# Kernel tuning notes

Hardware: AMD Instinct MI355X
Metric: run time of the kernel (lower is better)

Reference implementation:

```python
import jax, jax.numpy as jnp
import numpy as np

B, D, C, T = 2, 1024, 256, 32
H = 8
F = C // H
E = 1024  # time_embed_dim
GROUPS = 32
SCALE = F ** -0.5


def group_norm(x, scale, bias):
    # x: [B, D, C, T]; GroupNorm(32, C) over (channels-in-group, T)
    b, d, c, t = x.shape
    xg = x.reshape(b, d, GROUPS, c // GROUPS, t)
    m = xg.mean(axis=(3, 4), keepdims=True)
    v = xg.var(axis=(3, 4), keepdims=True)
    xn = ((xg - m) * jax.lax.rsqrt(v + 1e-5)).reshape(b, d, c, t)
    return xn * scale[None, None, :, None] + bias[None, None, :, None]


def rpe_R(temb, pairwise, dw, db, tw, tb, ow, ob):
    # pairwise: [B, T, T] int -> R: [B, T, T, H, F]
    pd = pairwise.astype(jnp.float32)
    dist_embs = jnp.stack([
        jnp.log1p(jnp.maximum(pd, 0.0)),
        jnp.log1p(jnp.maximum(-pd, 0.0)),
        (pairwise == 0).astype(jnp.float32),
    ], axis=-1)  # [B, T, T, 3]
    emb = (temb @ tw.T + tb)[:, :, None, :] + (dist_embs @ dw.T + db)  # [B,T,T,C]
    r = jax.nn.silu(emb) @ ow.T + ob
    return r.reshape(r.shape[0], r.shape[1], r.shape[2], H, F)


def setup_inputs() -> dict:
    key = jax.random.key(0)
    ks = jax.random.split(key, 20)
    s = 0.02
    inp = {
        "x": jax.random.normal(ks[0], (B, D, C, T), jnp.float32),
        "temb": jax.random.normal(ks[1], (B, T, E), jnp.float32),
        "norm_scale": jnp.ones((C,), jnp.float32),
        "norm_bias": jnp.zeros((C,), jnp.float32),
        "qkv_w": jax.random.normal(ks[2], (3 * C, C), jnp.float32) * s,
        "qkv_b": jnp.zeros((3 * C,), jnp.float32),
        "proj_w": jax.random.normal(ks[3], (C, C), jnp.float32) * s,
        "proj_b": jnp.zeros((C,), jnp.float32),
        # stacked RPE params for (q, k, v) nets
        "rpe_dist_w": jax.random.normal(ks[4], (3, C, 3), jnp.float32) * s,
        "rpe_dist_b": jnp.zeros((3, C), jnp.float32),
        "rpe_time_w": jax.random.normal(ks[5], (3, C, E), jnp.float32) * s,
        "rpe_time_b": jnp.zeros((3, C), jnp.float32),
        "rpe_out_w": jax.random.normal(ks[6], (3, C, C), jnp.float32) * s,
        "rpe_out_b": jax.random.normal(ks[7], (3, C), jnp.float32) * s,
        "frame_indices": jnp.sort(jax.random.randint(ks[8], (B, T), 0, 100), axis=-1),
    }
    return inp


def reference(x, temb, norm_scale, norm_bias, qkv_w, qkv_b, proj_w, proj_b,
              rpe_dist_w, rpe_dist_b, rpe_time_w, rpe_time_b, rpe_out_w, rpe_out_b,
              frame_indices):
    xn = group_norm(x, norm_scale, norm_bias)          # [B,D,C,T]
    xt = jnp.einsum('BDCT->BDTC', xn)                  # [B,D,T,C]
    qkv = (xt @ qkv_w.T + qkv_b).reshape(B, D, T, 3, H, F)
    qkv = jnp.einsum('BDTtHF->tBDHTF', qkv)
    q, k, v = qkv[0] * SCALE, qkv[1], qkv[2]           # [B,D,H,T,F]

    attn = jnp.einsum('bdhtf,bdhsf->bdhts', q, k)

    pairwise = frame_indices[:, :, None] - frame_indices[:, None, :]  # [B,T,T]
    R_q = rpe_R(temb, pairwise, rpe_dist_w[0], rpe_dist_b[0], rpe_time_w[0], rpe_time_b[0], rpe_out_w[0], rpe_out_b[0])
    R_k = rpe_R(temb, pairwise, rpe_dist_w[1], rpe_dist_b[1], rpe_time_w[1], rpe_time_b[1], rpe_out_w[1], rpe_out_b[1])
    R_v = rpe_R(temb, pairwise, rpe_dist_w[2], rpe_dist_b[2], rpe_time_w[2], rpe_time_b[2], rpe_out_w[2], rpe_out_b[2])

    attn = attn + jnp.einsum('bdhtf,btshf->bdhts', q, R_k)
    # rpe_q: forward_qk on (k*scale) then transpose last two dims
    attn = attn + jnp.einsum('bdhtf,btshf->bdhts', k * SCALE, R_q).swapaxes(-1, -2)

    attn = jax.nn.softmax(attn.astype(jnp.float32), axis=-1).astype(attn.dtype)

    out = jnp.einsum('bdhts,bdhsf->bdhtf', attn, v)
    out = out + jnp.einsum('bdhts,btshf->bdhtf', attn, R_v)

    out = jnp.einsum('BDHTF->BDTHF', out).reshape(B, D, T, C)
    out = out @ proj_w.T + proj_b
    y = xt + out                                       # residual on post-norm x (as in source)
    return jnp.einsum('BDTC->BDCT', y)
```

## Files before the change

kernel.cpp:

```cpp
#include <hip/hip_runtime.h>

#define BB 2
#define DD 1024
#define CC 256
#define TT 32
#define HH 8
#define FF 32
#define EE 1024
#define SCALE 0.17677669529663687f

typedef unsigned short u16;
typedef unsigned int u32;
typedef __attribute__((ext_vector_type(8))) short s8v;
typedef __attribute__((ext_vector_type(4))) float f32x4;

static __device__ __forceinline__ float u2f(u16 u) {
  return __uint_as_float(((u32)u) << 16);
}
static __device__ __forceinline__ u16 f2u(float f) {
  u32 x = __float_as_uint(f);
  x += 0x7fffu + ((x >> 16) & 1u);
  return (u16)(x >> 16);
}
static __device__ __forceinline__ float dot2bf(u32 a, u32 b, float c) {
  float d;
  asm("v_dot2_f32_bf16 %0, %1, %2, %3" : "=v"(d) : "v"(a), "v"(b), "v"(c));
  return d;
}
#define D2(acc, a, b) acc = dot2bf(a, b, acc)

static __device__ __forceinline__ float logits_r(
    const u16* kr,
    uint4 r0, uint4 r1, uint4 r2, uint4 r3,
    uint4 r4, uint4 r5, uint4 r6, uint4 r7,
    uint4 q0, uint4 q1, uint4 q2, uint4 q3) {
  uint4 k0 = *(const uint4*)(kr + 0);
  uint4 k1 = *(const uint4*)(kr + 8);
  uint4 k2 = *(const uint4*)(kr + 16);
  uint4 k3 = *(const uint4*)(kr + 24);
  float xq = 0.f, xr = 0.f, xk = 0.f;
  D2(xq, q0.x, k0.x); D2(xq, q0.y, k0.y); D2(xq, q0.z, k0.z); D2(xq, q0.w, k0.w);
  D2(xq, q1.x, k1.x); D2(xq, q1.y, k1.y); D2(xq, q1.z, k1.z); D2(xq, q1.w, k1.w);
  D2(xq, q2.x, k2.x); D2(xq, q2.y, k2.y); D2(xq, q2.z, k2.z); D2(xq, q2.w, k2.w);
  D2(xq, q3.x, k3.x); D2(xq, q3.y, k3.y); D2(xq, q3.z, k3.z); D2(xq, q3.w, k3.w);
  D2(xr, q0.x, r0.x); D2(xr, q0.y, r0.y); D2(xr, q0.z, r0.z); D2(xr, q0.w, r0.w);
  D2(xr, q1.x, r1.x); D2(xr, q1.y, r1.y); D2(xr, q1.z, r1.z); D2(xr, q1.w, r1.w);
  D2(xr, q2.x, r2.x); D2(xr, q2.y, r2.y); D2(xr, q2.z, r2.z); D2(xr, q2.w, r2.w);
  D2(xr, q3.x, r3.x); D2(xr, q3.y, r3.y); D2(xr, q3.z, r3.z); D2(xr, q3.w, r3.w);
  D2(xk, k0.x, r4.x); D2(xk, k0.y, r4.y); D2(xk, k0.z, r4.z); D2(xk, k0.w, r4.w);
  D2(xk, k1.x, r5.x); D2(xk, k1.y, r5.y); D2(xk, k1.z, r5.z); D2(xk, k1.w, r5.w);
  D2(xk, k2.x, r6.x); D2(xk, k2.y, r6.y); D2(xk, k2.z, r6.z); D2(xk, k2.w, r6.w);
  D2(xk, k3.x, r7.x); D2(xk, k3.y, r7.y); D2(xk, k3.z, r7.z); D2(xk, k3.w, r7.w);
  return xq + xr + xk;
}

static __device__ __forceinline__ float pv_r(
    uint4 p0, uint4 p1, uint4 p2, uint4 p3,
    const u16* vr, uint4 r0, uint4 r1, uint4 r2, uint4 r3) {
  uint4 v0 = *(const uint4*)(vr + 0),  v1 = *(const uint4*)(vr + 8);
  uint4 v2 = *(const uint4*)(vr + 16), v3 = *(const uint4*)(vr + 24);
  float o = 0.f;
  D2(o, p0.x, v0.x); D2(o, p0.y, v0.y); D2(o, p0.z, v0.z); D2(o, p0.w, v0.w);
  D2(o, p1.x, v1.x); D2(o, p1.y, v1.y); D2(o, p1.z, v1.z); D2(o, p1.w, v1.w);
  D2(o, p2.x, v2.x); D2(o, p2.y, v2.y); D2(o, p2.z, v2.z); D2(o, p2.w, v2.w);
  D2(o, p3.x, v3.x); D2(o, p3.y, v3.y); D2(o, p3.z, v3.z); D2(o, p3.w, v3.w);
  D2(o, p0.x, r0.x); D2(o, p0.y, r0.y); D2(o, p0.z, r0.z); D2(o, p0.w, r0.w);
  D2(o, p1.x, r1.x); D2(o, p1.y, r1.y); D2(o, p1.z, r1.z); D2(o, p1.w, r1.w);
  D2(o, p2.x, r2.x); D2(o, p2.y, r2.y); D2(o, p2.z, r2.z); D2(o, p2.w, r2.w);
  D2(o, p3.x, r3.x); D2(o, p3.y, r3.y); D2(o, p3.z, r3.z); D2(o, p3.w, r3.w);
  return o;
}

#define LOADROW8(P, v0, v1, v2, v3, v4, v5, v6, v7)                      \
  v0 = *(const uint4*)((P) + 0);  v1 = *(const uint4*)((P) + 8);         \
  v2 = *(const uint4*)((P) + 16); v3 = *(const uint4*)((P) + 24);        \
  v4 = *(const uint4*)((P) + 32); v5 = *(const uint4*)((P) + 40);        \
  v6 = *(const uint4*)((P) + 48); v7 = *(const uint4*)((P) + 56);
#define LOADROW4(P, v0, v1, v2, v3)                                      \
  v0 = *(const uint4*)((P) + 0);  v1 = *(const uint4*)((P) + 8);         \
  v2 = *(const uint4*)((P) + 16); v3 = *(const uint4*)((P) + 24);

__global__ void k_prep(const float* __restrict__ qw, const float* __restrict__ pw,
                       const float* __restrict__ ow, const float* __restrict__ tw,
                       u16* __restrict__ wpk2, u16* __restrict__ ppk,
                       u16* __restrict__ opk, float* __restrict__ twT) {
  int id = blockIdx.x * 256 + threadIdx.x;
  if (id < 24576) {
    int lane = id & 63, ks = (id >> 6) & 7, tile = id >> 9;
    int hh = tile / 6, r = tile % 6, sec = r >> 1, nt = r & 1;
    int nrow = sec * 256 + hh * 32 + nt * 16 + (lane & 15);
    int k = ks * 32 + (lane >> 4) * 8;
    const float* src = qw + (size_t)nrow * 256 + k;
    u16* dst = wpk2 + (size_t)id * 8;
#pragma unroll
    for (int e = 0; e < 8; ++e) dst[e] = f2u(src[e]);
  } else if (id < 32768) {
    int j = id - 24576;
    int lane = j & 63, ks = (j >> 6) & 7, nt = j >> 9;
    int row = nt * 16 + (lane & 15);
    int k = ks * 32 + (lane >> 4) * 8;
    const float* src = pw + (size_t)row * 256 + k;
    u16* dst = ppk + (size_t)j * 8;
#pragma unroll
    for (int e = 0; e < 8; ++e) dst[e] = f2u(src[e]);
  } else if (id < 57344) {
    int j = id - 32768;
    int lane = j & 63, ks = (j >> 6) & 7, g = j >> 9;
    int n = g >> 4, ntg = g & 15;
    int row = ntg * 16 + (lane & 15);
    int k = ks * 32 + (lane >> 4) * 8;
    const float* src = ow + ((size_t)n * 256 + row) * 256 + k;
    u16* dst = opk + (size_t)j * 8;
#pragma unroll
    for (int e = 0; e < 8; ++e) dst[e] = f2u(src[e]);
  } else {
    int j = id - 57344;
    int n = j >> 16, r = j & 65535;
    int e = r >> 6, c0 = (r & 63) * 4;
    float4 v;
    v.x = tw[((size_t)n * 256 + c0 + 0) * 1024 + e];
    v.y = tw[((size_t)n * 256 + c0 + 1) * 1024 + e];
    v.z = tw[((size_t)n * 256 + c0 + 2) * 1024 + e];
    v.w = tw[((size_t)n * 256 + c0 + 3) * 1024 + e];
    *(float4*)(twT + (size_t)n * 262144 + (size_t)e * 256 + c0) = v;
  }
}

__global__ __launch_bounds__(256) void k_tpe(
    const float* __restrict__ temb, const float* __restrict__ twT,
    const float* __restrict__ tb, const float* __restrict__ dw,
    const float* __restrict__ db, const int* __restrict__ fidx,
    u16* __restrict__ E) {
  int bid = blockIdx.x;
  int t = bid & 31, b = (bid >> 5) & 1, n = bid >> 6;
  __shared__ float st[EE];
  __shared__ int sfi[TT];
  for (int e = threadIdx.x; e < EE; e += 256)
    st[e] = temb[((size_t)b * TT + t) * EE + e];
  if (threadIdx.x < TT) sfi[threadIdx.x] = fidx[b * TT + threadIdx.x];
  __syncthreads();
  int c = threadIdx.x;
  const float* wp = twT + (size_t)n * 262144 + c;
  float a0 = 0.f, a1 = 0.f, a2 = 0.f, a3 = 0.f;
  for (int e = 0; e < EE; e += 4) {
    a0 += st[e + 0] * wp[(size_t)(e + 0) * 256];
    a1 += st[e + 1] * wp[(size_t)(e + 1) * 256];
    a2 += st[e + 2] * wp[(size_t)(e + 2) * 256];
    a3 += st[e + 3] * wp[(size_t)(e + 3) * 256];
  }
  float base = a0 + a1 + a2 + a3 + tb[n * 256 + c] + db[n * 256 + c];
  float dw0 = dw[(n * 256 + c) * 3 + 0];
  float dw1 = dw[(n * 256 + c) * 3 + 1];
  float dw2 = dw[(n * 256 + c) * 3 + 2];
  int ft = sfi[t];
  u16* erow = E + ((size_t)n * 2048 + b * 1024 + t * 32) * 256 + c;
  for (int s = 0; s < TT; ++s) {
    int pd = ft - sfi[s];
    float d0 = log1pf((float)(pd > 0 ? pd : 0));
    float d1 = log1pf((float)(pd < 0 ? -pd : 0));
    float d2 = (pd == 0) ? 1.f : 0.f;
    float e = base + d0 * dw0 + d1 * dw1 + d2 * dw2;
    float se = e / (1.f + expf(-e));
    erow[(size_t)s * 256] = f2u(se);
  }
}

__global__ __launch_bounds__(256) void k_rgemm(
    const u16* __restrict__ E, const u16* __restrict__ opk,
    const float* __restrict__ ob,
    u16* __restrict__ RKQ, u16* __restrict__ Rv) {
  int bid = blockIdx.x;
  int n = bid >> 6, rem = bid & 63;
  int mblk = rem >> 1, nblk = rem & 1;
  int tid = threadIdx.x;
  int w = tid >> 6, lane = tid & 63;
  int l15 = lane & 15, l4 = lane >> 4;
  size_t rowbase = (size_t)n * 2048 + mblk * 64;

  f32x4 acc[2][4];
#pragma unroll
  for (int i = 0; i < 2; ++i) {
    int ntg = nblk * 8 + w * 2 + i;
    float ov = ob[n * 256 + ntg * 16 + l15];
#pragma unroll
    for (int mt = 0; mt < 4; ++mt) acc[i][mt] = (f32x4){ov, ov, ov, ov};
  }
  for (int ks = 0; ks < 8; ++ks) {
    s8v a[4];
#pragma unroll
    for (int mt = 0; mt < 4; ++mt)
      a[mt] = *(const s8v*)(E + (rowbase + mt * 16 + l15) * 256 + ks * 32 + l4 * 8);
#pragma unroll
    for (int i = 0; i < 2; ++i) {
      int ntg = nblk * 8 + w * 2 + i;
      s8v bf = *(const s8v*)(opk + (((size_t)(n * 16 + ntg) * 8 + ks) * 64 + lane) * 8);
#pragma unroll
      for (int mt = 0; mt < 4; ++mt)
        acc[i][mt] = __builtin_amdgcn_mfma_f32_16x16x32_bf16(a[mt], bf, acc[i][mt], 0, 0, 0);
    }
  }
#pragma unroll
  for (int i = 0; i < 2; ++i) {
    int cc = (nblk * 8 + w * 2 + i) * 16 + l15;
    int hh = cc >> 5, f = cc & 31;
#pragma unroll
    for (int mt = 0; mt < 4; ++mt)
#pragma unroll
      for (int r = 0; r < 4; ++r) {
        int rloc = mblk * 64 + mt * 16 + l4 * 4 + r;
        int bb2 = rloc >> 10, tt = (rloc >> 5) & 31, ss = rloc & 31;
        size_t bh = (size_t)(bb2 * 8 + hh);
        float v = acc[i][mt][r];
        if (n == 0)      RKQ[(bh * 1024 + ss * 32 + tt) * 64 + 32 + f] = f2u(v * SCALE);
        else if (n == 1) RKQ[(bh * 1024 + tt * 32 + ss) * 64 + f] = f2u(v);
        else             Rv[((bh * 32 + tt) * 32 + f) * 32 + ss] = f2u(v);
      }
  }
}

__global__ __launch_bounds__(256, 4) void k_gn(
    const float* __restrict__ x, const float* __restrict__ nsc,
    const float* __restrict__ nbi, u16* __restrict__ pun) {
  int bid = blockIdx.x;
  int xcd = bid & 7, jj = bid >> 3;
  int b = xcd >> 2;
  int d = (xcd & 3) * 256 + jj;
  const int tid = threadIdx.x;
  __shared__ u16 xt[TT][264];
  const size_t xbase = ((size_t)(b * DD + d)) * 8192;
  u16* xnp = pun + xbase * 2 + 8192;
  {
    const int c0 = tid >> 3, tq = tid & 7;
    for (int c = c0; c < CC; c += 32) {
      float4 v = *(const float4*)(x + xbase + (size_t)c * TT + tq * 4);
      xt[tq * 4 + 0][c] = f2u(v.x);
      xt[tq * 4 + 1][c] = f2u(v.y);
      xt[tq * 4 + 2][c] = f2u(v.z);
      xt[tq * 4 + 3][c] = f2u(v.w);
    }
  }
  __syncthreads();
  {
    const int c = tid;
    float s = 0.f, s2 = 0.f;
    for (int t = 0; t < TT; ++t) { float v = u2f(xt[t][c]); s += v; s2 += v * v; }
    s += __shfl_xor(s, 1); s2 += __shfl_xor(s2, 1);
    s += __shfl_xor(s, 2); s2 += __shfl_xor(s2, 2);
    s += __shfl_xor(s, 4); s2 += __shfl_xor(s2, 4);
    const float mean = s * (1.f / 256.f);
    const float var = s2 * (1.f / 256.f) - mean * mean;
    const float rs = rsqrtf(var + 1e-5f);
    const float scv = nsc[c] * rs;
    const float biv = nbi[c] - mean * scv;
    for (int t = 0; t < TT; ++t) xt[t][c] = f2u(u2f(xt[t][c]) * scv + biv);
  }
  __syncthreads();
#pragma unroll
  for (int it = 0; it < 4; ++it) {
    int u = it * 256 + tid;
    int t = u >> 5, c = (u & 31) * 8;
    *(uint4*)(xnp + (size_t)u * 8) = *(const uint4*)&xt[t][c];
  }
}

__global__ __launch_bounds__(256, 3) void k_attn(
    u16* __restrict__ pun, const u16* __restrict__ wpk2,
    const float* __restrict__ qkb,
    const u16* __restrict__ RKQ, const u16* __restrict__ Rv) {
  int bid = blockIdx.x;
  int xcd = bid & 7, i5 = bid >> 3;
  int b = xcd >> 2;
  int h = i5 & 7;
  int dg = (xcd & 3) * 64 + (i5 >> 3);
  int d0 = dg * 4;
  const int tid = threadIdx.x;
  __shared__ u16 xsbuf[32 * 264];
  __shared__ u16 qs[4][32][40];
  __shared__ u16 ks_[4][32][40];
  __shared__ u16 vT[4][32][40];
#define XS_(r, c)   xsbuf[(r) * 264 + (c)]
#define ATSP(d, t)  (xsbuf + ((d) * 32 + (t)) * 40)

  const int w = tid >> 6, lane = tid & 63;
  const int l15 = lane & 15, l4 = lane >> 4;
  const int t = tid >> 3, j = tid & 7;
  const size_t bh = (size_t)(b * 8 + h);
  const u16* rp0 = RKQ + (bh * 1024 + (size_t)t * 32 + j) * 64;
  const u16* rv0 = Rv + ((bh * 32 + (size_t)t) * 32 + j) * 32;

  u16* slot0 = pun + ((size_t)(b * DD + d0)) * 16384;

  const u16* xp0 = slot0 + 8192;
  uint4 xr0 = *(const uint4*)(xp0 + (size_t)tid * 8);
  uint4 xr1 = *(const uint4*)(xp0 + (size_t)(256 + tid) * 8);
  uint4 xr2 = *(const uint4*)(xp0 + (size_t)(512 + tid) * 8);
  uint4 xr3 = *(const uint4*)(xp0 + (size_t)(768 + tid) * 8);

  for (int d = 0; d < 4; ++d) {
    *(uint4*)&XS_((tid >> 5), (tid & 31) * 8) = xr0;
    *(uint4*)&XS_(8 + (tid >> 5), (tid & 31) * 8) = xr1;
    *(uint4*)&XS_(16 + (tid >> 5), (tid & 31) * 8) = xr2;
    *(uint4*)&XS_(24 + (tid >> 5), (tid & 31) * 8) = xr3;
    __syncthreads();
    if (d < 3) {
      const u16* nx = slot0 + (size_t)(d + 1) * 16384 + 8192;
      xr0 = *(const uint4*)(nx + (size_t)tid * 8);
      xr1 = *(const uint4*)(nx + (size_t)(256 + tid) * 8);
      xr2 = *(const uint4*)(nx + (size_t)(512 + tid) * 8);
      xr3 = *(const uint4*)(nx + (size_t)(768 + tid) * 8);
    }
#pragma unroll
    for (int i = 0; i < 3; ++i) {
      const int u = w * 3 + i;
      const int sec = u >> 2;
      const int nt = (u >> 1) & 1;
      const int mh = u & 1;
      f32x4 acc = {0.f, 0.f, 0.f, 0.f};
      const u16* wb = wpk2 + ((size_t)((h * 6 + sec * 2 + nt) * 8) * 64 + lane) * 8;
      for (int ks = 0; ks < 8; ++ks) {
        s8v a = *(const s8v*)&XS_(mh * 16 + l15, ks * 32 + l4 * 8);
        s8v bf = *(const s8v*)(wb + (size_t)ks * 512);
        acc = __builtin_amdgcn_mfma_f32_16x16x32_bf16(a, bf, acc, 0, 0, 0);
      }
      const int f = nt * 16 + l15;
      const float bias = qkb[sec * 256 + h * 32 + f];
#pragma unroll
      for (int r = 0; r < 4; ++r) {
        const int tt = mh * 16 + l4 * 4 + r;
        const float val = acc[r] + bias;
        if (sec == 0)      qs[d][tt][f] = f2u(val * SCALE);
        else if (sec == 1) ks_[d][tt][f] = f2u(val);
        else               vT[d][f][tt] = f2u(val);
      }
    }
    __syncthreads();
  }

  uint4 q[4][4];
#pragma unroll
  for (int d = 0; d < 4; ++d) {
    q[d][0] = *(const uint4*)&qs[d][t][0];
    q[d][1] = *(const uint4*)&qs[d][t][8];
    q[d][2] = *(const uint4*)&qs[d][t][16];
    q[d][3] = *(const uint4*)&qs[d][t][24];
  }
  float a[4][4];
  uint4 A0, A1, A2, A3, A4, A5, A6, A7;
  uint4 B0, B1, B2, B3, B4, B5, B6, B7;
  LOADROW8(rp0,          A0, A1, A2, A3, A4, A5, A6, A7)
  LOADROW8(rp0 + 8 * 64, B0, B1, B2, B3, B4, B5, B6, B7)
#pragma unroll
  for (int d = 0; d < 4; ++d)
    a[d][0] = logits_r(&ks_[d][j][0], A0, A1, A2, A3, A4, A5, A6, A7,
                       q[d][0], q[d][1], q[d][2], q[d][3]);
  LOADROW8(rp0 + 16 * 64, A0, A1, A2, A3, A4, A5, A6, A7)
#pragma unroll
  for (int d = 0; d < 4; ++d)
    a[d][1] = logits_r(&ks_[d][j + 8][0], B0, B1, B2, B3, B4, B5, B6, B7,
                       q[d][0], q[d][1], q[d][2], q[d][3]);
  LOADROW8(rp0 + 24 * 64, B0, B1, B2, B3, B4, B5, B6, B7)
#pragma unroll
  for (int d = 0; d < 4; ++d)
    a[d][2] = logits_r(&ks_[d][j + 16][0], A0, A1, A2, A3, A4, A5, A6, A7,
                       q[d][0], q[d][1], q[d][2], q[d][3]);
#pragma unroll
  for (int d = 0; d < 4; ++d)
    a[d][3] = logits_r(&ks_[d][j + 24][0], B0, B1, B2, B3, B4, B5, B6, B7,
                       q[d][0], q[d][1], q[d][2], q[d][3]);

#pragma unroll
  for (int d = 0; d < 4; ++d) {
    float mx = fmaxf(fmaxf(a[d][0], a[d][1]), fmaxf(a[d][2], a[d][3]));
    mx = fmaxf(mx, __shfl_xor(mx, 1));
    mx = fmaxf(mx, __shfl_xor(mx, 2));
    mx = fmaxf(mx, __shfl_xor(mx, 4));
    float e0 = __expf(a[d][0] - mx), e1 = __expf(a[d][1] - mx);
    float e2 = __expf(a[d][2] - mx), e3 = __expf(a[d][3] - mx);
    float sum = e0 + e1 + e2 + e3;
    sum += __shfl_xor(sum, 1);
    sum += __shfl_xor(sum, 2);
    sum += __shfl_xor(sum, 4);
    const float inv = 1.f / sum;
    u16* ap = ATSP(d, t);
    ap[j]      = f2u(e0 * inv);
    ap[j + 8]  = f2u(e1 * inv);
    ap[j + 16] = f2u(e2 * inv);
    ap[j + 24] = f2u(e3 * inv);
  }

  uint4 p[4][4];
#pragma unroll
  for (int d = 0; d < 4; ++d) {
    const u16* ap = ATSP(d, t);
    p[d][0] = *(const uint4*)(ap + 0);
    p[d][1] = *(const uint4*)(ap + 8);
    p[d][2] = *(const uint4*)(ap + 16);
    p[d][3] = *(const uint4*)(ap + 24);
  }
  float o[4][4];
  uint4 VA0, VA1, VA2, VA3, VB0, VB1, VB2, VB3;
  LOADROW4(rv0,          VA0, VA1, VA2, VA3)
  LOADROW4(rv0 + 8 * 32, VB0, VB1, VB2, VB3)
#pragma unroll
  for (int d = 0; d < 4; ++d)
    o[d][0] = pv_r(p[d][0], p[d][1], p[d][2], p[d][3], &vT[d][j][0],
                   VA0, VA1, VA2, VA3);
  LOADROW4(rv0 + 16 * 32, VA0, VA1, VA2, VA3)
#pragma unroll
  for (int d = 0; d < 4; ++d)
    o[d][1] = pv_r(p[d][0], p[d][1], p[d][2], p[d][3], &vT[d][j + 8][0],
                   VB0, VB1, VB2, VB3);
  LOADROW4(rv0 + 24 * 32, VB0, VB1, VB2, VB3)
#pragma unroll
  for (int d = 0; d < 4; ++d)
    o[d][2] = pv_r(p[d][0], p[d][1], p[d][2], p[d][3], &vT[d][j + 16][0],
                   VA0, VA1, VA2, VA3);
#pragma unroll
  for (int d = 0; d < 4; ++d)
    o[d][3] = pv_r(p[d][0], p[d][1], p[d][2], p[d][3], &vT[d][j + 24][0],
                   VB0, VB1, VB2, VB3);

#pragma unroll
  for (int d = 0; d < 4; ++d) {
    u16* op = slot0 + (size_t)d * 16384 + (size_t)t * 256 + h * 32 + j;
    op[0]  = f2u(o[d][0]);
    op[8]  = f2u(o[d][1]);
    op[16] = f2u(o[d][2]);
    op[24] = f2u(o[d][3]);
  }
#undef XS_
#undef ATSP
}

__global__ __launch_bounds__(256, 4) void k_proj(
    u16* __restrict__ pun, const u16* __restrict__ ppk,
    const float* __restrict__ pb, float* __restrict__ out) {
  int bid = blockIdx.x;
  int xcd = bid & 7, jj = bid >> 3;
  int b = xcd >> 2;
  int d = (xcd & 3) * 256 + jj;
  const int tid = threadIdx.x;
  __shared__ u16 obuf[32][264];
  __shared__ u16 xs[32][264];
  const size_t nbase = ((size_t)(b * DD + d)) * 8192;
  u16* slot = pun + nbase * 2;
#pragma unroll
  for (int it = 0; it < 4; ++it) {
    int u = it * 256 + tid;
    int t = u >> 5, c = (u & 31) * 8;
    *(uint4*)&obuf[t][c] = *(const uint4*)(slot + (size_t)u * 8);
    *(uint4*)&xs[t][c]   = *(const uint4*)(slot + 8192 + (size_t)u * 8);
  }
  __syncthreads();

  const int w = tid >> 6, lane = tid & 63;
  const int l15 = lane & 15, l4 = lane >> 4;
  f32x4 pacc[4][2];
#pragma unroll
  for (int i = 0; i < 4; ++i) {
    pacc[i][0] = (f32x4){0.f, 0.f, 0.f, 0.f};
    pacc[i][1] = (f32x4){0.f, 0.f, 0.f, 0.f};
  }
  for (int ks = 0; ks < 8; ++ks) {
    s8v a0 = *(const s8v*)&obuf[l15][ks * 32 + l4 * 8];
    s8v a1 = *(const s8v*)&obuf[16 + l15][ks * 32 + l4 * 8];
#pragma unroll
    for (int i = 0; i < 4; ++i) {
      s8v bf = *(const s8v*)(ppk + ((size_t)((w * 4 + i) * 8 + ks) * 64 + lane) * 8);
      pacc[i][0] = __builtin_amdgcn_mfma_f32_16x16x32_bf16(a0, bf, pacc[i][0], 0, 0, 0);
      pacc[i][1] = __builtin_amdgcn_mfma_f32_16x16x32_bf16(a1, bf, pacc[i][1], 0, 0, 0);
    }
  }
#pragma unroll
  for (int i = 0; i < 4; ++i) {
    const int co = (w * 4 + i) * 16 + l15;
    const float pbv = pb[co];
#pragma unroll
    for (int mt = 0; mt < 2; ++mt) {
      const int t0 = mt * 16 + l4 * 4;
      float4 sv;
      sv.x = pacc[i][mt][0] + u2f(xs[t0 + 0][co]) + pbv;
      sv.y = pacc[i][mt][1] + u2f(xs[t0 + 1][co]) + pbv;
      sv.z = pacc[i][mt][2] + u2f(xs[t0 + 2][co]) + pbv;
      sv.w = pacc[i][mt][3] + u2f(xs[t0 + 3][co]) + pbv;
      *(float4*)(out + nbase + (size_t)co * TT + t0) = sv;
    }
  }
}

extern "C" void kernel_launch(void* const* d_in, const int* in_sizes, int n_in,
                              void* d_out, int out_size, void* d_ws, size_t ws_size,
                              hipStream_t stream) {
  const float* x      = (const float*)d_in[0];
  const float* temb   = (const float*)d_in[1];
  const float* nsc    = (const float*)d_in[2];
  const float* nbi    = (const float*)d_in[3];
  const float* qkv_w  = (const float*)d_in[4];
  const float* qkv_b  = (const float*)d_in[5];
  const float* proj_w = (const float*)d_in[6];
  const float* proj_b = (const float*)d_in[7];
  const float* dw     = (const float*)d_in[8];
  const float* db     = (const float*)d_in[9];
  const float* tw     = (const float*)d_in[10];
  const float* tb     = (const float*)d_in[11];
  const float* ow     = (const float*)d_in[12];
  const float* ob     = (const float*)d_in[13];
  const int*   fidx   = (const int*)d_in[14];
  float* out = (float*)d_out;
  u16* pun = (u16*)d_out;

  float* twT = (float*)d_ws;
  u16* wpk2 = (u16*)(twT + 786432);
  u16* ppk  = wpk2 + 196608;
  u16* opk  = ppk + 65536;
  u16* E    = opk + 196608;
  u16* RKQ  = E + 1572864;
  u16* Rv   = RKQ + 1048576;

  k_prep<<<992, 256, 0, stream>>>(qkv_w, proj_w, ow, tw, wpk2, ppk, opk, twT);
  k_tpe<<<192, 256, 0, stream>>>(temb, twT, tb, dw, db, fidx, E);
  k_rgemm<<<192, 256, 0, stream>>>(E, opk, ob, RKQ, Rv);
  k_gn<<<2048, 256, 0, stream>>>(x, nsc, nbi, pun);
  k_attn<<<4096, 256, 0, stream>>>(pun, wpk2, qkv_b, RKQ, Rv);
  k_proj<<<2048, 256, 0, stream>>>(pun, ppk, proj_b, out);
}
```

Before: 249.0 us.

## Fuse prep, time-embedding and groupnorm kernels; prefetch RPE rows in attention

Merges weight packing, the time-embedding projection and groupnorm into a single launch partitioned by block index. This removes two launches and lets the independent stages run concurrently. The time-embedding dot product now reads tw directly with coalesced row-wise float4 loads and a shuffle reduction, which drops the transposed twT copy and its workspace. In the attention kernel, the first RPE row loads are issued before the QKV projection loop, pinned in registers with empty asm barriers, and q and p are reloaded from shared memory instead of held in registers, trading register pressure for LDS traffic.

```diff
diff --git a/kernel.cpp b/kernel.cpp
--- a/kernel.cpp
+++ b/kernel.cpp
@@ -28,16 +28,16 @@
   return d;
 }
 #define D2(acc, a, b) acc = dot2bf(a, b, acc)
-
-static __device__ __forceinline__ float logits_r(
-    const u16* kr,
+#define KEEP4(v) asm volatile("" : "+v"(v.x), "+v"(v.y), "+v"(v.z), "+v"(v.w))
+
+static __device__ __forceinline__ float logits_q(
+    const u16* kr, const u16* qr,
     uint4 r0, uint4 r1, uint4 r2, uint4 r3,
-    uint4 r4, uint4 r5, uint4 r6, uint4 r7,
-    uint4 q0, uint4 q1, uint4 q2, uint4 q3) {
-  uint4 k0 = *(const uint4*)(kr + 0);
-  uint4 k1 = *(const uint4*)(kr + 8);
-  uint4 k2 = *(const uint4*)(kr + 16);
-  uint4 k3 = *(const uint4*)(kr + 24);
+    uint4 r4, uint4 r5, uint4 r6, uint4 r7) {
+  uint4 q0 = *(const uint4*)(qr + 0),  q1 = *(const uint4*)(qr + 8);
+  uint4 q2 = *(const uint4*)(qr + 16), q3 = *(const uint4*)(qr + 24);
+  uint4 k0 = *(const uint4*)(kr + 0),  k1 = *(const uint4*)(kr + 8);
+  uint4 k2 = *(const uint4*)(kr + 16), k3 = *(const uint4*)(kr + 24);
   float xq = 0.f, xr = 0.f, xk = 0.f;
   D2(xq, q0.x, k0.x); D2(xq, q0.y, k0.y); D2(xq, q0.z, k0.z); D2(xq, q0.w, k0.w);
   D2(xq, q1.x, k1.x); D2(xq, q1.y, k1.y); D2(xq, q1.z, k1.z); D2(xq, q1.w, k1.w);
@@ -54,9 +54,11 @@
   return xq + xr + xk;
 }
 
-static __device__ __forceinline__ float pv_r(
-    uint4 p0, uint4 p1, uint4 p2, uint4 p3,
-    const u16* vr, uint4 r0, uint4 r1, uint4 r2, uint4 r3) {
+static __device__ __forceinline__ float pv_q(
+    const u16* pr, const u16* vr,
+    uint4 r0, uint4 r1, uint4 r2, uint4 r3) {
+  uint4 p0 = *(const uint4*)(pr + 0),  p1 = *(const uint4*)(pr + 8);
+  uint4 p2 = *(const uint4*)(pr + 16), p3 = *(const uint4*)(pr + 24);
   uint4 v0 = *(const uint4*)(vr + 0),  v1 = *(const uint4*)(vr + 8);
   uint4 v2 = *(const uint4*)(vr + 16), v3 = *(const uint4*)(vr + 24);
   float o = 0.f;
@@ -79,89 +81,135 @@
 #define LOADROW4(P, v0, v1, v2, v3)                                      \
   v0 = *(const uint4*)((P) + 0);  v1 = *(const uint4*)((P) + 8);         \
   v2 = *(const uint4*)((P) + 16); v3 = *(const uint4*)((P) + 24);
-
-__global__ void k_prep(const float* __restrict__ qw, const float* __restrict__ pw,
-                       const float* __restrict__ ow, const float* __restrict__ tw,
-                       u16* __restrict__ wpk2, u16* __restrict__ ppk,
-                       u16* __restrict__ opk, float* __restrict__ twT) {
-  int id = blockIdx.x * 256 + threadIdx.x;
-  if (id < 24576) {
-    int lane = id & 63, ks = (id >> 6) & 7, tile = id >> 9;
-    int hh = tile / 6, r = tile % 6, sec = r >> 1, nt = r & 1;
-    int nrow = sec * 256 + hh * 32 + nt * 16 + (lane & 15);
-    int k = ks * 32 + (lane >> 4) * 8;
-    const float* src = qw + (size_t)nrow * 256 + k;
-    u16* dst = wpk2 + (size_t)id * 8;
-#pragma unroll
-    for (int e = 0; e < 8; ++e) dst[e] = f2u(src[e]);
-  } else if (id < 32768) {
-    int j = id - 24576;
-    int lane = j & 63, ks = (j >> 6) & 7, nt = j >> 9;
-    int row = nt * 16 + (lane & 15);
-    int k = ks * 32 + (lane >> 4) * 8;
-    const float* src = pw + (size_t)row * 256 + k;
-    u16* dst = ppk + (size_t)j * 8;
-#pragma unroll
-    for (int e = 0; e < 8; ++e) dst[e] = f2u(src[e]);
-  } else if (id < 57344) {
-    int j = id - 32768;
-    int lane = j & 63, ks = (j >> 6) & 7, g = j >> 9;
-    int n = g >> 4, ntg = g & 15;
-    int row = ntg * 16 + (lane & 15);
-    int k = ks * 32 + (lane >> 4) * 8;
-    const float* src = ow + ((size_t)n * 256 + row) * 256 + k;
-    u16* dst = opk + (size_t)j * 8;
-#pragma unroll
-    for (int e = 0; e < 8; ++e) dst[e] = f2u(src[e]);
+#define KEEP8(a0,a1,a2,a3,a4,a5,a6,a7) \
+  KEEP4(a0); KEEP4(a1); KEEP4(a2); KEEP4(a3); KEEP4(a4); KEEP4(a5); KEEP4(a6); KEEP4(a7)
+
+__global__ __launch_bounds__(256, 4) void k_f0(
+    const float* __restrict__ x, const float* __restrict__ nsc,
+    const float* __restrict__ nbi, u16* __restrict__ pun,
+    const float* __restrict__ qw, const float* __restrict__ pw,
+    const float* __restrict__ ow, const float* __restrict__ tw,
+    const float* __restrict__ temb, const float* __restrict__ tb,
+    const float* __restrict__ dw, const float* __restrict__ db,
+    const int* __restrict__ fidx,
+    u16* __restrict__ wpk2, u16* __restrict__ ppk, u16* __restrict__ opk,
+    u16* __restrict__ E) {
+  const int bid = blockIdx.x;
+  const int tid = threadIdx.x;
+  __shared__ u16 xt[TT][264];
+  __shared__ float st[EE];
+  __shared__ float base_s[CC];
+  __shared__ int sfi[TT];
+
+  if (bid < 2048) {
+    int xcd = bid & 7, jj = bid >> 3;
+    int b = xcd >> 2;
+    int d = (xcd & 3) * 256 + jj;
+    const size_t xbase = ((size_t)(b * DD + d)) * 8192;
+    u16* xnp = pun + xbase * 2 + 8192;
+    {
+      const int c0 = tid >> 3, tq = tid & 7;
+      for (int c = c0; c < CC; c += 32) {
+        float4 v = *(const float4*)(x + xbase + (size_t)c * TT + tq * 4);
+        xt[tq * 4 + 0][c] = f2u(v.x);
+        xt[tq * 4 + 1][c] = f2u(v.y);
+        xt[tq * 4 + 2][c] = f2u(v.z);
+        xt[tq * 4 + 3][c] = f2u(v.w);
+      }
+    }
+    __syncthreads();
+    {
+      const int c = tid;
+      float s = 0.f, s2 = 0.f;
+      for (int t = 0; t < TT; ++t) { float v = u2f(xt[t][c]); s += v; s2 += v * v; }
+      s += __shfl_xor(s, 1); s2 += __shfl_xor(s2, 1);
+      s += __shfl_xor(s, 2); s2 += __shfl_xor(s2, 2);
+      s += __shfl_xor(s, 4); s2 += __shfl_xor(s2, 4);
+      const float mean = s * (1.f / 256.f);
+      const float var = s2 * (1.f / 256.f) - mean * mean;
+      const float rs = rsqrtf(var + 1e-5f);
+      const float scv = nsc[c] * rs;
+      const float biv = nbi[c] - mean * scv;
+      for (int t = 0; t < TT; ++t) xt[t][c] = f2u(u2f(xt[t][c]) * scv + biv);
+    }
+    __syncthreads();
+#pragma unroll
+    for (int it = 0; it < 4; ++it) {
+      int u = it * 256 + tid;
+      int t = u >> 5, c = (u & 31) * 8;
+      *(uint4*)(xnp + (size_t)u * 8) = *(const uint4*)&xt[t][c];
+    }
+  } else if (bid < 2272) {
+    int id = (bid - 2048) * 256 + tid;
+    if (id < 24576) {
+      int lane = id & 63, ks = (id >> 6) & 7, tile = id >> 9;
+      int hh = tile / 6, r = tile % 6, sec = r >> 1, nt = r & 1;
+      int nrow = sec * 256 + hh * 32 + nt * 16 + (lane & 15);
+      int k = ks * 32 + (lane >> 4) * 8;
+      const float* src = qw + (size_t)nrow * 256 + k;
+      u16* dst = wpk2 + (size_t)id * 8;
+#pragma unroll
+      for (int e = 0; e < 8; ++e) dst[e] = f2u(src[e]);
+    } else if (id < 32768) {
+      int j = id - 24576;
+      int lane = j & 63, ks = (j >> 6) & 7, nt = j >> 9;
+      int row = nt * 16 + (lane & 15);
+      int k = ks * 32 + (lane >> 4) * 8;
+      const float* src = pw + (size_t)row * 256 + k;
+      u16* dst = ppk + (size_t)j * 8;
+#pragma unroll
+      for (int e = 0; e < 8; ++e) dst[e] = f2u(src[e]);
+    } else {
+      int j = id - 32768;
+      int lane = j & 63, ks = (j >> 6) & 7, g = j >> 9;
+      int n = g >> 4, ntg = g & 15;
+      int row = ntg * 16 + (lane & 15);
+      int k = ks * 32 + (lane >> 4) * 8;
+      const float* src = ow + ((size_t)n * 256 + row) * 256 + k;
+      u16* dst = opk + (size_t)j * 8;
+#pragma unroll
+      for (int e = 0; e < 8; ++e) dst[e] = f2u(src[e]);
+    }
   } else {
-    int j = id - 57344;
-    int n = j >> 16, r = j & 65535;
-    int e = r >> 6, c0 = (r & 63) * 4;
-    float4 v;
-    v.x = tw[((size_t)n * 256 + c0 + 0) * 1024 + e];
-    v.y = tw[((size_t)n * 256 + c0 + 1) * 1024 + e];
-    v.z = tw[((size_t)n * 256 + c0 + 2) * 1024 + e];
-    v.w = tw[((size_t)n * 256 + c0 + 3) * 1024 + e];
-    *(float4*)(twT + (size_t)n * 262144 + (size_t)e * 256 + c0) = v;
-  }
-}
-
-__global__ __launch_bounds__(256) void k_tpe(
-    const float* __restrict__ temb, const float* __restrict__ twT,
-    const float* __restrict__ tb, const float* __restrict__ dw,
-    const float* __restrict__ db, const int* __restrict__ fidx,
-    u16* __restrict__ E) {
-  int bid = blockIdx.x;
-  int t = bid & 31, b = (bid >> 5) & 1, n = bid >> 6;
-  __shared__ float st[EE];
-  __shared__ int sfi[TT];
-  for (int e = threadIdx.x; e < EE; e += 256)
-    st[e] = temb[((size_t)b * TT + t) * EE + e];
-  if (threadIdx.x < TT) sfi[threadIdx.x] = fidx[b * TT + threadIdx.x];
-  __syncthreads();
-  int c = threadIdx.x;
-  const float* wp = twT + (size_t)n * 262144 + c;
-  float a0 = 0.f, a1 = 0.f, a2 = 0.f, a3 = 0.f;
-  for (int e = 0; e < EE; e += 4) {
-    a0 += st[e + 0] * wp[(size_t)(e + 0) * 256];
-    a1 += st[e + 1] * wp[(size_t)(e + 1) * 256];
-    a2 += st[e + 2] * wp[(size_t)(e + 2) * 256];
-    a3 += st[e + 3] * wp[(size_t)(e + 3) * 256];
-  }
-  float base = a0 + a1 + a2 + a3 + tb[n * 256 + c] + db[n * 256 + c];
-  float dw0 = dw[(n * 256 + c) * 3 + 0];
-  float dw1 = dw[(n * 256 + c) * 3 + 1];
-  float dw2 = dw[(n * 256 + c) * 3 + 2];
-  int ft = sfi[t];
-  u16* erow = E + ((size_t)n * 2048 + b * 1024 + t * 32) * 256 + c;
-  for (int s = 0; s < TT; ++s) {
-    int pd = ft - sfi[s];
-    float d0 = log1pf((float)(pd > 0 ? pd : 0));
-    float d1 = log1pf((float)(pd < 0 ? -pd : 0));
-    float d2 = (pd == 0) ? 1.f : 0.f;
-    float e = base + d0 * dw0 + d1 * dw1 + d2 * dw2;
-    float se = e / (1.f + expf(-e));
-    erow[(size_t)s * 256] = f2u(se);
+    int bid3 = bid - 2272;
+    int t = bid3 & 31, b = (bid3 >> 5) & 1, n = bid3 >> 6;
+    for (int e = tid; e < EE; e += 256)
+      st[e] = temb[((size_t)b * TT + t) * EE + e];
+    if (tid < TT) sfi[tid] = fidx[b * TT + tid];
+    __syncthreads();
+    const int g = tid & 7, cl = tid >> 3;
+#pragma unroll
+    for (int pass = 0; pass < 8; ++pass) {
+      const int c = pass * 32 + cl;
+      const float* wr = tw + ((size_t)n * 256 + c) * 1024 + g * 4;
+      float acc = 0.f;
+      for (int step = 0; step < 32; ++step) {
+        float4 wv = *(const float4*)(wr + step * 32);
+        float4 sv = *(const float4*)(st + g * 4 + step * 32);
+        acc += sv.x * wv.x + sv.y * wv.y + sv.z * wv.z + sv.w * wv.w;
+      }
+      acc += __shfl_xor(acc, 1);
+      acc += __shfl_xor(acc, 2);
+      acc += __shfl_xor(acc, 4);
+      if (g == 0) base_s[c] = acc;
+    }
+    __syncthreads();
+    const int c = tid;
+    float base = base_s[c] + tb[n * 256 + c] + db[n * 256 + c];
+    float dw0 = dw[(n * 256 + c) * 3 + 0];
+    float dw1 = dw[(n * 256 + c) * 3 + 1];
+    float dw2 = dw[(n * 256 + c) * 3 + 2];
+    int ft = sfi[t];
+    u16* erow = E + ((size_t)n * 2048 + b * 1024 + t * 32) * 256 + c;
+    for (int s = 0; s < TT; ++s) {
+      int pd = ft - sfi[s];
+      float d0 = log1pf((float)(pd > 0 ? pd : 0));
+      float d1 = log1pf((float)(pd < 0 ? -pd : 0));
+      float d2 = (pd == 0) ? 1.f : 0.f;
+      float e = base + d0 * dw0 + d1 * dw1 + d2 * dw2;
+      float se = e / (1.f + expf(-e));
+      erow[(size_t)s * 256] = f2u(se);
+    }
   }
 }
 
@@ -215,51 +263,6 @@
         else if (n == 1) RKQ[(bh * 1024 + tt * 32 + ss) * 64 + f] = f2u(v);
         else             Rv[((bh * 32 + tt) * 32 + f) * 32 + ss] = f2u(v);
       }
-  }
-}
-
-__global__ __launch_bounds__(256, 4) void k_gn(
-    const float* __restrict__ x, const float* __restrict__ nsc,
-    const float* __restrict__ nbi, u16* __restrict__ pun) {
-  int bid = blockIdx.x;
-  int xcd = bid & 7, jj = bid >> 3;
-  int b = xcd >> 2;
-  int d = (xcd & 3) * 256 + jj;
-  const int tid = threadIdx.x;
-  __shared__ u16 xt[TT][264];
-  const size_t xbase = ((size_t)(b * DD + d)) * 8192;
-  u16* xnp = pun + xbase * 2 + 8192;
-  {
-    const int c0 = tid >> 3, tq = tid & 7;
-    for (int c = c0; c < CC; c += 32) {
-      float4 v = *(const float4*)(x + xbase + (size_t)c * TT + tq * 4);
-      xt[tq * 4 + 0][c] = f2u(v.x);
-      xt[tq * 4 + 1][c] = f2u(v.y);
-      xt[tq * 4 + 2][c] = f2u(v.z);
-      xt[tq * 4 + 3][c] = f2u(v.w);
-    }
-  }
-  __syncthreads();
-  {
-    const int c = tid;
-    float s = 0.f, s2 = 0.f;
-    for (int t = 0; t < TT; ++t) { float v = u2f(xt[t][c]); s += v; s2 += v * v; }
-    s += __shfl_xor(s, 1); s2 += __shfl_xor(s2, 1);
-    s += __shfl_xor(s, 2); s2 += __shfl_xor(s2, 2);
-    s += __shfl_xor(s, 4); s2 += __shfl_xor(s2, 4);
-    const float mean = s * (1.f / 256.f);
-    const float var = s2 * (1.f / 256.f) - mean * mean;
-    const float rs = rsqrtf(var + 1e-5f);
-    const float scv = nsc[c] * rs;
-    const float biv = nbi[c] - mean * scv;
-    for (int t = 0; t < TT; ++t) xt[t][c] = f2u(u2f(xt[t][c]) * scv + biv);
-  }
-  __syncthreads();
-#pragma unroll
-  for (int it = 0; it < 4; ++it) {
-    int u = it * 256 + tid;
-    int t = u >> 5, c = (u & 31) * 8;
-    *(uint4*)(xnp + (size_t)u * 8) = *(const uint4*)&xt[t][c];
   }
 }
 
@@ -296,6 +299,18 @@
   uint4 xr2 = *(const uint4*)(xp0 + (size_t)(512 + tid) * 8);
   uint4 xr3 = *(const uint4*)(xp0 + (size_t)(768 + tid) * 8);
 
+  uint4 A0, A1, A2, A3, A4, A5, A6, A7;
+  uint4 B0, B1, B2, B3, B4, B5, B6, B7;
+  uint4 VA0, VA1, VA2, VA3, VB0, VB1, VB2, VB3;
+  LOADROW8(rp0,          A0, A1, A2, A3, A4, A5, A6, A7)
+  LOADROW8(rp0 + 8 * 64, B0, B1, B2, B3, B4, B5, B6, B7)
+  LOADROW4(rv0,          VA0, VA1, VA2, VA3)
+  LOADROW4(rv0 + 8 * 32, VB0, VB1, VB2, VB3)
+  KEEP8(A0, A1, A2, A3, A4, A5, A6, A7);
+  KEEP8(B0, B1, B2, B3, B4, B5, B6, B7);
+  KEEP4(VA0); KEEP4(VA1); KEEP4(VA2); KEEP4(VA3);
+  KEEP4(VB0); KEEP4(VB1); KEEP4(VB2); KEEP4(VB3);
+
   for (int d = 0; d < 4; ++d) {
     *(uint4*)&XS_((tid >> 5), (tid & 31) * 8) = xr0;
     *(uint4*)&XS_(8 + (tid >> 5), (tid & 31) * 8) = xr1;
@@ -336,37 +351,27 @@
     __syncthreads();
   }
 
-  uint4 q[4][4];
-#pragma unroll
-  for (int d = 0; d < 4; ++d) {
-    q[d][0] = *(const uint4*)&qs[d][t][0];
-    q[d][1] = *(const uint4*)&qs[d][t][8];
-    q[d][2] = *(const uint4*)&qs[d][t][16];
-    q[d][3] = *(const uint4*)&qs[d][t][24];
-  }
   float a[4][4];
-  uint4 A0, A1, A2, A3, A4, A5, A6, A7;
-  uint4 B0, B1, B2, B3, B4, B5, B6, B7;
-  LOADROW8(rp0,          A0, A1, A2, A3, A4, A5, A6, A7)
-  LOADROW8(rp0 + 8 * 64, B0, B1, B2, B3, B4, B5, B6, B7)
-#pragma unroll
-  for (int d = 0; d < 4; ++d)
-    a[d][0] = logits_r(&ks_[d][j][0], A0, A1, A2, A3, A4, A5, A6, A7,
-                       q[d][0], q[d][1], q[d][2], q[d][3]);
+#pragma unroll
+  for (int d = 0; d < 4; ++d)
+    a[d][0] = logits_q(&ks_[d][j][0], &qs[d][t][0],
+                       A0, A1, A2, A3, A4, A5, A6, A7);
   LOADROW8(rp0 + 16 * 64, A0, A1, A2, A3, A4, A5, A6, A7)
-#pragma unroll
-  for (int d = 0; d < 4; ++d)
-    a[d][1] = logits_r(&ks_[d][j + 8][0], B0, B1, B2, B3, B4, B5, B6, B7,
-                       q[d][0], q[d][1], q[d][2], q[d][3]);
+  KEEP8(A0, A1, A2, A3, A4, A5, A6, A7);
+#pragma unroll
+  for (int d = 0; d < 4; ++d)
+    a[d][1] = logits_q(&ks_[d][j + 8][0], &qs[d][t][0],
+                       B0, B1, B2, B3, B4, B5, B6, B7);
   LOADROW8(rp0 + 24 * 64, B0, B1, B2, B3, B4, B5, B6, B7)
-#pragma unroll
-  for (int d = 0; d < 4; ++d)
-    a[d][2] = logits_r(&ks_[d][j + 16][0], A0, A1, A2, A3, A4, A5, A6, A7,
-                       q[d][0], q[d][1], q[d][2], q[d][3]);
-#pragma unroll
-  for (int d = 0; d < 4; ++d)
-    a[d][3] = logits_r(&ks_[d][j + 24][0], B0, B1, B2, B3, B4, B5, B6, B7,
-                       q[d][0], q[d][1], q[d][2], q[d][3]);
+  KEEP8(B0, B1, B2, B3, B4, B5, B6, B7);
+#pragma unroll
+  for (int d = 0; d < 4; ++d)
+    a[d][2] = logits_q(&ks_[d][j + 16][0], &qs[d][t][0],
+                       A0, A1, A2, A3, A4, A5, A6, A7);
+#pragma unroll
+  for (int d = 0; d < 4; ++d)
+    a[d][3] = logits_q(&ks_[d][j + 24][0], &qs[d][t][0],
+                       B0, B1, B2, B3, B4, B5, B6, B7);
 
 #pragma unroll
   for (int d = 0; d < 4; ++d) {
@@ -388,37 +393,23 @@
     ap[j + 24] = f2u(e3 * inv);
   }
 
-  uint4 p[4][4];
-#pragma unroll
-  for (int d = 0; d < 4; ++d) {
-    const u16* ap = ATSP(d, t);
-    p[d][0] = *(const uint4*)(ap + 0);
-    p[d][1] = *(const uint4*)(ap + 8);
-    p[d][2] = *(const uint4*)(ap + 16);
-    p[d][3] = *(const uint4*)(ap + 24);
-  }
   float o[4][4];
-  uint4 VA0, VA1, VA2, VA3, VB0, VB1, VB2, VB3;
-  LOADROW4(rv0,          VA0, VA1, VA2, VA3)
-  LOADROW4(rv0 + 8 * 32, VB0, VB1, VB2, VB3)
-#pragma unroll
-  for (int d = 0; d < 4; ++d)
-    o[d][0] = pv_r(p[d][0], p[d][1], p[d][2], p[d][3], &vT[d][j][0],
-                   VA0, VA1, VA2, VA3);
+#pragma unroll
+  for (int d = 0; d < 4; ++d)
+    o[d][0] = pv_q(ATSP(d, t), &vT[d][j][0], VA0, VA1, VA2, VA3);
   LOADROW4(rv0 + 16 * 32, VA0, VA1, VA2, VA3)
-#pragma unroll
-  for (int d = 0; d < 4; ++d)
-    o[d][1] = pv_r(p[d][0], p[d][1], p[d][2], p[d][3], &vT[d][j + 8][0],
-                   VB0, VB1, VB2, VB3);
+  KEEP4(VA0); KEEP4(VA1); KEEP4(VA2); KEEP4(VA3);
+#pragma unroll
+  for (int d = 0; d < 4; ++d)
+    o[d][1] = pv_q(ATSP(d, t), &vT[d][j + 8][0], VB0, VB1, VB2, VB3);
   LOADROW4(rv0 + 24 * 32, VB0, VB1, VB2, VB3)
-#pragma unroll
-  for (int d = 0; d < 4; ++d)
-    o[d][2] = pv_r(p[d][0], p[d][1], p[d][2], p[d][3], &vT[d][j + 16][0],
-                   VA0, VA1, VA2, VA3);
-#pragma unroll
-  for (int d = 0; d < 4; ++d)
-    o[d][3] = pv_r(p[d][0], p[d][1], p[d][2], p[d][3], &vT[d][j + 24][0],
-                   VB0, VB1, VB2, VB3);
+  KEEP4(VB0); KEEP4(VB1); KEEP4(VB2); KEEP4(VB3);
+#pragma unroll
+  for (int d = 0; d < 4; ++d)
+    o[d][2] = pv_q(ATSP(d, t), &vT[d][j + 16][0], VA0, VA1, VA2, VA3);
+#pragma unroll
+  for (int d = 0; d < 4; ++d)
+    o[d][3] = pv_q(ATSP(d, t), &vT[d][j + 24][0], VB0, VB1, VB2, VB3);
 
 #pragma unroll
   for (int d = 0; d < 4; ++d) {
@@ -509,18 +500,16 @@
   float* out = (float*)d_out;
   u16* pun = (u16*)d_out;
 
-  float* twT = (float*)d_ws;
-  u16* wpk2 = (u16*)(twT + 786432);
+  u16* wpk2 = (u16*)d_ws;
   u16* ppk  = wpk2 + 196608;
   u16* opk  = ppk + 65536;
   u16* E    = opk + 196608;
   u16* RKQ  = E + 1572864;
   u16* Rv   = RKQ + 1048576;
 
-  k_prep<<<992, 256, 0, stream>>>(qkv_w, proj_w, ow, tw, wpk2, ppk, opk, twT);
-  k_tpe<<<192, 256, 0, stream>>>(temb, twT, tb, dw, db, fidx, E);
+  k_f0<<<2464, 256, 0, stream>>>(x, nsc, nbi, pun, qkv_w, proj_w, ow, tw,
+                                 temb, tb, dw, db, fidx, wpk2, ppk, opk, E);
   k_rgemm<<<192, 256, 0, stream>>>(E, opk, ob, RKQ, Rv);
-  k_gn<<<2048, 256, 0, stream>>>(x, nsc, nbi, pun);
   k_attn<<<4096, 256, 0, stream>>>(pun, wpk2, qkv_b, RKQ, Rv);
   k_proj<<<2048, 256, 0, stream>>>(pun, ppk, proj_b, out);
 }
```

After: 413.6 us. 1.66x slower.
